# Kernel tuning notes

Hardware: AMD Instinct MI355X
Metric: run time of the kernel (lower is better)

## Reference

```python
import jax, jax.numpy as jnp
import numpy as np
import math

B, S, D = 4, 2048, 1024
H, DK, DV = 16, 64, 64

def setup_inputs() -> dict:
    key = jax.random.key(0)
    ks = jax.random.split(key, 8)
    query = jax.random.normal(ks[0], (B, S, D), dtype=jnp.float32)
    key_t = jax.random.normal(ks[1], (B, S, D), dtype=jnp.float32)
    value = jax.random.normal(ks[2], (B, S, D), dtype=jnp.float32)
    # causal mask: True = masked (filled with -inf), broadcast over [B,H,S,S]
    mask = jnp.triu(jnp.ones((S, S), dtype=bool), k=1)[None, None, :, :]
    s = 0.02
    w_q = jax.random.normal(ks[3], (D, H * DK), dtype=jnp.float32) * s
    w_k = jax.random.normal(ks[4], (D, H * DK), dtype=jnp.float32) * s
    w_v = jax.random.normal(ks[5], (D, H * DV), dtype=jnp.float32) * s
    w_o = jax.random.normal(ks[6], (H * DV, D), dtype=jnp.float32) * s
    return {"query": query, "key": key_t, "value": value, "mask": mask,
            "w_q": w_q, "w_k": w_k, "w_v": w_v, "w_o": w_o}

def reference(query, key, value, mask, w_q, w_k, w_v, w_o):
    b, s, _ = query.shape
    # projections -> [B, H, S, dk/dv]
    q = (query @ w_q).reshape(b, s, H, DK).transpose(0, 2, 1, 3)
    k = (key @ w_k).reshape(b, s, H, DK).transpose(0, 2, 1, 3)
    v = (value @ w_v).reshape(b, s, H, DV).transpose(0, 2, 1, 3)
    scores = jnp.einsum('bhqd,bhkd->bhqk', q, k) / math.sqrt(DK)
    scores = jnp.where(mask, -jnp.inf, scores)
    attn = jax.nn.softmax(scores, axis=-1)
    out = jnp.einsum('bhqk,bhkd->bhqd', attn, v)
    out = out.transpose(0, 2, 1, 3).reshape(b, s, H * DV)
    return out @ w_o
```

## Files before the change

kernel.cpp:

```cpp
#include <hip/hip_runtime.h>
#include <hip/hip_bf16.h>

#define S_LEN 2048
#define NH 16
#define DHEAD 64
#define DMODEL 1024
#define BATCH 4

typedef __attribute__((ext_vector_type(4))) float f32x4;
typedef __attribute__((ext_vector_type(8))) short bf16x8;
typedef __attribute__((ext_vector_type(4))) short s16x4;
typedef __attribute__((ext_vector_type(4))) float fl4;
typedef __attribute__((ext_vector_type(4))) unsigned u32x4;

static __device__ __forceinline__ short f2bf(float f) {
  unsigned u = __builtin_bit_cast(unsigned, f);
  u += 0x7fffu + ((u >> 16) & 1u);
  return (short)(u >> 16);
}
static __device__ __forceinline__ f32x4 mfma16(bf16x8 a, bf16x8 b, f32x4 c) {
  return __builtin_amdgcn_mfma_f32_16x16x32_bf16(a, b, c, 0, 0, 0);
}
static __device__ __forceinline__ void gl_lds16(const short* g, short* l) {
  __builtin_amdgcn_global_load_lds(
      (const __attribute__((address_space(1))) unsigned*)g,
      (__attribute__((address_space(3))) unsigned*)l, 16, 0, 0);
}
static __device__ __forceinline__ unsigned cvt_pk_bf16(float lo, float hi) {
  unsigned r;
  asm("v_cvt_pk_bf16_f32 %0, %1, %2" : "=v"(r) : "v"(lo), "v"(hi));
  return r;
}

__global__ __launch_bounds__(256) void cvt_bf16(const float* __restrict__ src,
                                                short* __restrict__ dst) {
  const size_t i = ((size_t)blockIdx.x * 256 + threadIdx.x) * 8;
  fl4 a = *(const fl4*)(src + i);
  fl4 b = *(const fl4*)(src + i + 4);
  bf16x8 o;
  o[0] = f2bf(a.x); o[1] = f2bf(a.y); o[2] = f2bf(a.z); o[3] = f2bf(a.w);
  o[4] = f2bf(b.x); o[5] = f2bf(b.y); o[6] = f2bf(b.z); o[7] = f2bf(b.w);
  *(bf16x8*)(dst + i) = o;
}

__global__ __launch_bounds__(256) void transpose_w3(
    const float* __restrict__ w0, const float* __restrict__ w1,
    const float* __restrict__ w2, short* __restrict__ o0,
    short* __restrict__ o1, short* __restrict__ o2) {
  const float* W = blockIdx.z == 0 ? w0 : blockIdx.z == 1 ? w1 : w2;
  short* O = blockIdx.z == 0 ? o0 : blockIdx.z == 1 ? o1 : o2;
  __shared__ __align__(16) short T[64][72];
  const int tid = threadIdx.x;
  const int k0 = blockIdx.y * 64, n0 = blockIdx.x * 64;
#pragma unroll
  for (int i = 0; i < 4; ++i) {
    int c = tid + i * 256;
    int kk = c >> 4, nn = (c & 15) << 2;
    fl4 v = *(const fl4*)(W + (size_t)(k0 + kk) * DMODEL + n0 + nn);
    T[nn + 0][kk] = f2bf(v.x);
    T[nn + 1][kk] = f2bf(v.y);
    T[nn + 2][kk] = f2bf(v.z);
    T[nn + 3][kk] = f2bf(v.w);
  }
  __syncthreads();
#pragma unroll
  for (int i = 0; i < 4; ++i) {
    int c = tid + i * 256;
    int nn = c >> 4, kk = (c & 15) << 2;
    *(s16x4*)(O + (size_t)(n0 + nn) * DMODEL + k0 + kk) = *(const s16x4*)&T[nn][kk];
  }
}

__global__ __launch_bounds__(256) void transpose_w1(
    const float* __restrict__ W, short* __restrict__ O) {
  __shared__ __align__(16) short T[64][72];
  const int tid = threadIdx.x;
  const int k0 = blockIdx.y * 64, n0 = blockIdx.x * 64;
#pragma unroll
  for (int i = 0; i < 4; ++i) {
    int c = tid + i * 256;
    int kk = c >> 4, nn = (c & 15) << 2;
    fl4 v = *(const fl4*)(W + (size_t)(k0 + kk) * DMODEL + n0 + nn);
    T[nn + 0][kk] = f2bf(v.x);
    T[nn + 1][kk] = f2bf(v.y);
    T[nn + 2][kk] = f2bf(v.z);
    T[nn + 3][kk] = f2bf(v.w);
  }
  __syncthreads();
#pragma unroll
  for (int i = 0; i < 4; ++i) {
    int c = tid + i * 256;
    int nn = c >> 4, kk = (c & 15) << 2;
    *(s16x4*)(O + (size_t)(n0 + nn) * DMODEL + k0 + kk) = *(const s16x4*)&T[nn][kk];
  }
}

template <int OUT_MODE>
__global__ __launch_bounds__(256) void gemm128(
    const short* __restrict__ A, const short* __restrict__ Bt,
    void* __restrict__ OutP, float scale) {
  __shared__ __align__(16) short As[128 * 32];
  __shared__ __align__(16) short Bs[128 * 32];
  const int tid = threadIdx.x, lane = tid & 63, wid = tid >> 6;
  const int m0 = blockIdx.x * 128, n0 = blockIdx.y * 128;
  const int wm = (wid >> 1) * 64, wn = (wid & 1) * 64;
  const int lr = lane & 15, g = lane >> 4, lk = g << 3;

  f32x4 acc[4][4] = {};

  const int srow = wid * 32 + (lane >> 2);
  const int scol = (lane & 3) * 8;
  short* ldsA = As + wid * 1024 + lane * 8;
  short* ldsB = Bs + wid * 1024 + lane * 8;

  for (int k0 = 0; k0 < DMODEL; k0 += 32) {
    __syncthreads();
    {
      const short* ga = A + (size_t)(m0 + srow) * DMODEL + k0 + scol;
      gl_lds16(ga, ldsA);
      gl_lds16(ga + (size_t)16 * DMODEL, ldsA + 512);
      const short* gb = Bt + (size_t)(n0 + srow) * DMODEL + k0 + scol;
      gl_lds16(gb, ldsB);
      gl_lds16(gb + (size_t)16 * DMODEL, ldsB + 512);
    }
    __syncthreads();

    bf16x8 af[4], bfr[4];
#pragma unroll
    for (int t = 0; t < 4; ++t) {
      af[t] = *(const bf16x8*)&As[(wm + t * 16 + lr) * 32 + lk];
      bfr[t] = *(const bf16x8*)&Bs[(wn + t * 16 + lr) * 32 + lk];
    }
#pragma unroll
    for (int mi = 0; mi < 4; ++mi)
#pragma unroll
      for (int ni = 0; ni < 4; ++ni)
        acc[mi][ni] = mfma16(af[mi], bfr[ni], acc[mi][ni]);
  }

  if (OUT_MODE == 0) {
    short* Out = (short*)OutP;
#pragma unroll
    for (int mi = 0; mi < 4; ++mi)
#pragma unroll
      for (int ni = 0; ni < 4; ++ni) {
        const int n = n0 + wn + ni * 16 + lr;
        const int h = n >> 6, d = n & 63;
#pragma unroll
        for (int r = 0; r < 4; ++r) {
          const int m = m0 + wm + mi * 16 + g * 4 + r;
          const int b = m >> 11, s = m & (S_LEN - 1);
          Out[(((size_t)b * NH + h) * S_LEN + s) * DHEAD + d] =
              f2bf(acc[mi][ni][r] * scale);
        }
      }
  } else if (OUT_MODE == 1) {
    short* Out = (short*)OutP;
#pragma unroll
    for (int mi = 0; mi < 4; ++mi) {
      const int mb = m0 + wm + mi * 16 + g * 4;
      const int b = mb >> 11, s = mb & (S_LEN - 1);
#pragma unroll
      for (int ni = 0; ni < 4; ++ni) {
        const int n = n0 + wn + ni * 16 + lr;
        const int h = n >> 6, d = n & 63;
        s16x4 pv;
        pv.x = f2bf(acc[mi][ni][0]);
        pv.y = f2bf(acc[mi][ni][1]);
        pv.z = f2bf(acc[mi][ni][2]);
        pv.w = f2bf(acc[mi][ni][3]);
        *(s16x4*)(Out + (((size_t)b * NH + h) * DHEAD + d) * S_LEN + s) = pv;
      }
    }
  } else {
    float* Out = (float*)OutP;
#pragma unroll
    for (int mi = 0; mi < 4; ++mi)
#pragma unroll
      for (int ni = 0; ni < 4; ++ni) {
        const int n = n0 + wn + ni * 16 + lr;
#pragma unroll
        for (int r = 0; r < 4; ++r) {
          const int m = m0 + wm + mi * 16 + g * 4 + r;
          Out[(size_t)m * DMODEL + n] = acc[mi][ni][r];
        }
      }
  }
}

static __device__ __forceinline__ void softmax_pf_static(
    f32x4 (&st)[4], bf16x8& pf0, bf16x8& pf1) {
#pragma unroll
  for (int nj = 0; nj < 4; ++nj)
#pragma unroll
    for (int r = 0; r < 4; ++r)
      st[nj][r] = exp2f(st[nj][r]);
  unsigned pw[2][4];
#pragma unroll
  for (int kc = 0; kc < 2; ++kc)
#pragma unroll
    for (int jj = 0; jj < 2; ++jj) {
      unsigned a = cvt_pk_bf16(st[2 * kc][2 * jj], st[2 * kc][2 * jj + 1]);
      unsigned bb = cvt_pk_bf16(st[2 * kc + 1][2 * jj], st[2 * kc + 1][2 * jj + 1]);
      asm("v_permlane32_swap_b32 %0, %1" : "+v"(a), "+v"(bb));
      asm("v_permlane16_swap_b32 %0, %1" : "+v"(a), "+v"(bb));
      pw[kc][jj] = a;
      pw[kc][jj + 2] = bb;
    }
  u32x4 w0 = {pw[0][0], pw[0][1], pw[0][2], pw[0][3]};
  u32x4 w1 = {pw[1][0], pw[1][1], pw[1][2], pw[1][3]};
  pf0 = __builtin_bit_cast(bf16x8, w0);
  pf1 = __builtin_bit_cast(bf16x8, w1);
}

static __device__ __forceinline__ void attn_epilogue(
    f32x4 (&ot)[4], float lsum, int b, int h, int qa, int g,
    short* __restrict__ AO) {
  const float inv = 1.f / lsum;
  short* dst = AO + ((size_t)b * S_LEN + qa) * DMODEL + h * DHEAD + (g << 2);
#pragma unroll
  for (int nd = 0; nd < 4; ++nd) {
    s16x4 pv;
    pv.x = f2bf(ot[nd][0] * inv);
    pv.y = f2bf(ot[nd][1] * inv);
    pv.z = f2bf(ot[nd][2] * inv);
    pv.w = f2bf(ot[nd][3] * inv);
    *(s16x4*)(dst + nd * 16) = pv;
  }
}

__global__ __launch_bounds__(256) void attn9(
    const short* __restrict__ Qp, const short* __restrict__ Kp,
    const short* __restrict__ VT, short* __restrict__ AO) {
  __shared__ __align__(16) short KV[2][8192];
  const int tid = threadIdx.x, lane = tid & 63, wid = tid >> 6;
  const int lr = lane & 15, g = lane >> 4;
  const int id = blockIdx.x;
  const int xcd = id & 7;
  const int bh = xcd * 8 + ((id >> 3) & 7);
  const int sg = 31 - (id >> 6);
  const int t = sg * 4 + wid;
  const short* Qb = Qp + (size_t)bh * S_LEN * DHEAD;
  const short* Kb = Kp + (size_t)bh * S_LEN * DHEAD;
  const short* Vb = VT + (size_t)bh * DHEAD * S_LEN;
  const int b = bh >> 4, h = bh & 15;

  const int NT = sg + 1;
  const int q0 = t << 4;
  const int qa = q0 + lr;

  const int row1 = tid >> 3;
  const int col1 = (tid & 7) ^ (row1 & 7);
  const int kOff1 = row1 * DHEAD + col1 * 8;
  const int vOff1 = row1 * S_LEN + col1 * 8;

#define STAGE9(bufi, kvv) do {                                      \
    const short* ks_ = Kb + (size_t)(kvv) * DHEAD + kOff1;          \
    gl_lds16(ks_,               &KV[bufi][0] + tid * 8);            \
    gl_lds16(ks_ + 32 * DHEAD,  &KV[bufi][2048] + tid * 8);         \
    const short* vs_ = Vb + (kvv) + vOff1;                          \
    gl_lds16(vs_,               &KV[bufi][4096] + tid * 8);         \
    gl_lds16(vs_ + 32 * S_LEN,  &KV[bufi][6144] + tid * 8);         \
  } while (0)

  const int slot0 = g ^ (lr & 7);
  const int fOff0 = lr * 64 + slot0 * 8;
  const int fOff1 = lr * 64 + (slot0 ^ 4) * 8;

  bf16x8 qf[2];
  qf[0] = *(const bf16x8*)(Qb + (size_t)qa * DHEAD + (g << 3));
  qf[1] = *(const bf16x8*)(Qb + (size_t)qa * DHEAD + 32 + (g << 3));

  bf16x8 ones;
#pragma unroll
  for (int i = 0; i < 8; ++i) ones[i] = (short)0x3F80;

  f32x4 ot[4] = {};
  f32x4 lacc = {};

  STAGE9(0, 0);

  for (int it = 0; it < NT; ++it) {
    const int kv0 = it << 6;
    const int cb = it & 1;
    if (it + 1 < NT) {
      STAGE9(cb ^ 1, kv0 + 64);
      asm volatile("s_waitcnt vmcnt(4)" ::: "memory");
    } else {
      asm volatile("s_waitcnt vmcnt(0)" ::: "memory");
    }
    __builtin_amdgcn_s_barrier();

    const short* kb = &KV[cb][0];
    const short* vb = &KV[cb][4096];

    f32x4 st[4] = {};
    __builtin_amdgcn_s_setprio(1);
#pragma unroll
    for (int nj = 0; nj < 4; ++nj) {
      bf16x8 k0 = *(const bf16x8*)(kb + fOff0 + nj * 1024);
      bf16x8 k1 = *(const bf16x8*)(kb + fOff1 + nj * 1024);
      st[nj] = mfma16(k0, qf[0], st[nj]);
      st[nj] = mfma16(k1, qf[1], st[nj]);
    }
    __builtin_amdgcn_s_setprio(0);
    if (it == NT - 1) {
#pragma unroll
      for (int nj = 0; nj < 4; ++nj)
#pragma unroll
        for (int r = 0; r < 4; ++r)
          if (kv0 + nj * 16 + (g << 2) + r > qa) st[nj][r] = -1e30f;
    }
    bf16x8 pf0, pf1;
    softmax_pf_static(st, pf0, pf1);
    __builtin_amdgcn_s_setprio(1);
    lacc = mfma16(ones, pf0, lacc);
    lacc = mfma16(ones, pf1, lacc);
#pragma unroll
    for (int nd = 0; nd < 4; ++nd) {
      bf16x8 v0 = *(const bf16x8*)(vb + fOff0 + nd * 1024);
      bf16x8 v1 = *(const bf16x8*)(vb + fOff1 + nd * 1024);
      ot[nd] = mfma16(v0, pf0, ot[nd]);
      ot[nd] = mfma16(v1, pf1, ot[nd]);
    }
    __builtin_amdgcn_s_setprio(0);
    __builtin_amdgcn_s_barrier();
  }
#undef STAGE9

  attn_epilogue(ot, lacc[0], b, h, qa, g, AO);
}

extern "C" void kernel_launch(void* const* d_in, const int* in_sizes, int n_in,
                              void* d_out, int out_size, void* d_ws, size_t ws_size,
                              hipStream_t stream) {
  const float* query = (const float*)d_in[0];
  const float* key   = (const float*)d_in[1];
  const float* value = (const float*)d_in[2];
  const float* w_q = (const float*)d_in[4];
  const float* w_k = (const float*)d_in[5];
  const float* w_v = (const float*)d_in[6];
  const float* w_o = (const float*)d_in[7];

  const size_t QKV = (size_t)BATCH * NH * S_LEN * DHEAD;
  short* Qp = (short*)d_ws;
  short* Kp = Qp + QKV;
  short* Vt = Kp + QKV;
  short* AO = Vt + QKV;
  short* Wto = Qp;
  short* qb  = (short*)d_out;
  short* Wtq = qb + QKV;
  short* Wtk = Wtq + (size_t)DMODEL * DMODEL;
  short* Wtv = Wtk + (size_t)DMODEL * DMODEL;

  dim3 blk(256);
  dim3 gg((BATCH * S_LEN) / 128, DMODEL / 128);
  const float qscale = 0.125f * 1.4426950408889634f;

  transpose_w3<<<dim3(16, 16, 3), blk, 0, stream>>>(w_q, w_k, w_v, Wtq, Wtk, Wtv);
  cvt_bf16<<<4096, blk, 0, stream>>>(query, qb);
  gemm128<0><<<gg, blk, 0, stream>>>(qb, Wtq, Qp, qscale);
  cvt_bf16<<<4096, blk, 0, stream>>>(key, qb);
  gemm128<0><<<gg, blk, 0, stream>>>(qb, Wtk, Kp, 1.0f);
  cvt_bf16<<<4096, blk, 0, stream>>>(value, qb);
  gemm128<1><<<gg, blk, 0, stream>>>(qb, Wtv, Vt, 1.0f);
  attn9<<<dim3(2048), blk, 0, stream>>>(Qp, Kp, Vt, AO);
  transpose_w1<<<dim3(16, 16), blk, 0, stream>>>(w_o, Wto);
  gemm128<2><<<gg, blk, 0, stream>>>(AO, Wto, d_out, 1.0f);
}
```

Measured before the change: 208.4 us.

## Double-buffer GEMM LDS loads and merge Q/K bf16 conversions

The GEMM main loop now uses two LDS buffers. The next k-slice's global-to-LDS loads are issued before computing on the current one, with vmcnt waits and raw barriers replacing the two __syncthreads, so load latency can overlap the MFMAs. LDS use per block doubles, which may lower occupancy. Separately, query and key are converted to bf16 in one launch, with key staged in the AO workspace so one kernel launch is saved.

```diff
diff --git a/kernel.cpp b/kernel.cpp
--- a/kernel.cpp
+++ b/kernel.cpp
@@ -30,6 +30,20 @@
   unsigned r;
   asm("v_cvt_pk_bf16_f32 %0, %1, %2" : "=v"(r) : "v"(lo), "v"(hi));
   return r;
+}
+
+__global__ __launch_bounds__(256) void cvt_qk2(
+    const float* __restrict__ q, const float* __restrict__ k,
+    short* __restrict__ oq, short* __restrict__ ok) {
+  const float* src = blockIdx.y ? k : q;
+  short* dst = blockIdx.y ? ok : oq;
+  const size_t i = ((size_t)blockIdx.x * 256 + threadIdx.x) * 8;
+  fl4 a = *(const fl4*)(src + i);
+  fl4 b = *(const fl4*)(src + i + 4);
+  bf16x8 o;
+  o[0] = f2bf(a.x); o[1] = f2bf(a.y); o[2] = f2bf(a.z); o[3] = f2bf(a.w);
+  o[4] = f2bf(b.x); o[5] = f2bf(b.y); o[6] = f2bf(b.z); o[7] = f2bf(b.w);
+  *(bf16x8*)(dst + i) = o;
 }
 
 __global__ __launch_bounds__(256) void cvt_bf16(const float* __restrict__ src,
@@ -99,8 +113,8 @@
 __global__ __launch_bounds__(256) void gemm128(
     const short* __restrict__ A, const short* __restrict__ Bt,
     void* __restrict__ OutP, float scale) {
-  __shared__ __align__(16) short As[128 * 32];
-  __shared__ __align__(16) short Bs[128 * 32];
+  __shared__ __align__(16) short As[2][128 * 32];
+  __shared__ __align__(16) short Bs[2][128 * 32];
   const int tid = threadIdx.x, lane = tid & 63, wid = tid >> 6;
   const int m0 = blockIdx.x * 128, n0 = blockIdx.y * 128;
   const int wm = (wid >> 1) * 64, wn = (wid & 1) * 64;
@@ -110,33 +124,43 @@
 
   const int srow = wid * 32 + (lane >> 2);
   const int scol = (lane & 3) * 8;
-  short* ldsA = As + wid * 1024 + lane * 8;
-  short* ldsB = Bs + wid * 1024 + lane * 8;
-
-  for (int k0 = 0; k0 < DMODEL; k0 += 32) {
-    __syncthreads();
-    {
-      const short* ga = A + (size_t)(m0 + srow) * DMODEL + k0 + scol;
-      gl_lds16(ga, ldsA);
-      gl_lds16(ga + (size_t)16 * DMODEL, ldsA + 512);
-      const short* gb = Bt + (size_t)(n0 + srow) * DMODEL + k0 + scol;
-      gl_lds16(gb, ldsB);
-      gl_lds16(gb + (size_t)16 * DMODEL, ldsB + 512);
-    }
-    __syncthreads();
+  const int ldsOff = wid * 1024 + lane * 8;
+
+#define GSTAGE(bufi, kk0) do {                                          \
+    const short* ga_ = A + (size_t)(m0 + srow) * DMODEL + (kk0) + scol; \
+    gl_lds16(ga_,                       &As[bufi][ldsOff]);             \
+    gl_lds16(ga_ + (size_t)16 * DMODEL, &As[bufi][ldsOff + 512]);       \
+    const short* gb_ = Bt + (size_t)(n0 + srow) * DMODEL + (kk0) + scol;\
+    gl_lds16(gb_,                       &Bs[bufi][ldsOff]);             \
+    gl_lds16(gb_ + (size_t)16 * DMODEL, &Bs[bufi][ldsOff + 512]);       \
+  } while (0)
+
+  GSTAGE(0, 0);
+  int it = 0;
+  for (int k0 = 0; k0 < DMODEL; k0 += 32, ++it) {
+    const int cb = it & 1;
+    if (k0 + 32 < DMODEL) {
+      GSTAGE(cb ^ 1, k0 + 32);
+      asm volatile("s_waitcnt vmcnt(4)" ::: "memory");
+    } else {
+      asm volatile("s_waitcnt vmcnt(0)" ::: "memory");
+    }
+    __builtin_amdgcn_s_barrier();
 
     bf16x8 af[4], bfr[4];
 #pragma unroll
     for (int t = 0; t < 4; ++t) {
-      af[t] = *(const bf16x8*)&As[(wm + t * 16 + lr) * 32 + lk];
-      bfr[t] = *(const bf16x8*)&Bs[(wn + t * 16 + lr) * 32 + lk];
+      af[t] = *(const bf16x8*)&As[cb][(wm + t * 16 + lr) * 32 + lk];
+      bfr[t] = *(const bf16x8*)&Bs[cb][(wn + t * 16 + lr) * 32 + lk];
     }
 #pragma unroll
     for (int mi = 0; mi < 4; ++mi)
 #pragma unroll
       for (int ni = 0; ni < 4; ++ni)
         acc[mi][ni] = mfma16(af[mi], bfr[ni], acc[mi][ni]);
-  }
+    __builtin_amdgcn_s_barrier();
+  }
+#undef GSTAGE
 
   if (OUT_MODE == 0) {
     short* Out = (short*)OutP;
@@ -358,11 +382,10 @@
   const float qscale = 0.125f * 1.4426950408889634f;
 
   transpose_w3<<<dim3(16, 16, 3), blk, 0, stream>>>(w_q, w_k, w_v, Wtq, Wtk, Wtv);
-  cvt_bf16<<<4096, blk, 0, stream>>>(query, qb);
+  cvt_qk2<<<dim3(4096, 2), blk, 0, stream>>>(query, key, qb, AO);
   gemm128<0><<<gg, blk, 0, stream>>>(qb, Wtq, Qp, qscale);
-  cvt_bf16<<<4096, blk, 0, stream>>>(key, qb);
-  gemm128<0><<<gg, blk, 0, stream>>>(qb, Wtk, Kp, 1.0f);
   cvt_bf16<<<4096, blk, 0, stream>>>(value, qb);
+  gemm128<0><<<gg, blk, 0, stream>>>(AO, Wtk, Kp, 1.0f);
   gemm128<1><<<gg, blk, 0, stream>>>(qb, Wtv, Vt, 1.0f);
   attn9<<<dim3(2048), blk, 0, stream>>>(Qp, Kp, Vt, AO);
   transpose_w1<<<dim3(16, 16), blk, 0, stream>>>(w_o, Wto);
```

Result: slower. 221.8 us (+6.4%).
